# Kernel optimization log

Measured on AMD Instinct MI355X. Metric: run time of the kernel, lower is better.

## Reference

```python
import jax, jax.numpy as jnp
import numpy as np

IMG = 512
SIZES = (16, 32, 64, 128, 256)
FEAT_HW = (128, 64, 32, 16, 8)
STRIDES = tuple(IMG // h for h in FEAT_HW)
RATIOS = np.array([0.5, 1.0, 2.0])
PRE_NMS = 1000        # pre_nms_top_n['testing']
POST_NMS = 300        # post_nms_top_n['testing']
NMS_THRESH = 0.7
MIN_SIZE = 1e-3
BBOX_XFORM_CLIP = float(np.log(1000.0 / 16.0))


def _base_anchors(size):
    h_r = np.sqrt(RATIOS)
    w_r = 1.0 / h_r
    ws = w_r * size
    hs = h_r * size
    return np.round(np.stack([-ws, -hs, ws, hs], axis=1) / 2.0)  # [3,4]


def _level_anchors(size, stride, hw):
    ba = _base_anchors(size)
    s = np.arange(hw, dtype=np.float32) * stride
    yy, xx = np.meshgrid(s, s, indexing='ij')  # y-major like torchvision
    shifts = np.stack([xx.ravel(), yy.ravel(), xx.ravel(), yy.ravel()], axis=1)
    return (shifts[:, None, :] + ba[None, :, :]).reshape(-1, 4).astype(np.float32)


ANCHORS = [jnp.asarray(_level_anchors(SIZES[i], STRIDES[i], FEAT_HW[i])) for i in range(5)]


def _conv(x, w, b, pad):
    y = jax.lax.conv_general_dilated(x, w, (1, 1), [(pad, pad), (pad, pad)],
                                     dimension_numbers=('NCHW', 'OIHW', 'NCHW'))
    return y + b[None, :, None, None]


def _decode(deltas, anchors):
    # deltas [N,K,4], anchors [K,4]; BoxCoder weights (1,1,1,1)
    w = anchors[:, 2] - anchors[:, 0]
    h = anchors[:, 3] - anchors[:, 1]
    cx = anchors[:, 0] + 0.5 * w
    cy = anchors[:, 1] + 0.5 * h
    dx, dy = deltas[..., 0], deltas[..., 1]
    dw = jnp.minimum(deltas[..., 2], BBOX_XFORM_CLIP)
    dh = jnp.minimum(deltas[..., 3], BBOX_XFORM_CLIP)
    pcx = dx * w + cx
    pcy = dy * h + cy
    pw = jnp.exp(dw) * w
    ph = jnp.exp(dh) * h
    return jnp.stack([pcx - 0.5 * pw, pcy - 0.5 * ph,
                      pcx + 0.5 * pw, pcy + 0.5 * ph], axis=-1)


def _nms_single(boxes_off, scores_masked, boxes_raw, scores_raw):
    # greedy NMS over fixed POST_NMS steps; suppressed/invalid score = -1
    def step(s, _):
        i = jnp.argmax(s)
        ok = s[i] > -0.5
        b = boxes_off[i]
        lt = jnp.maximum(b[:2], boxes_off[:, :2])
        rb = jnp.minimum(b[2:], boxes_off[:, 2:])
        wh = jnp.clip(rb - lt, 0.0)
        inter = wh[:, 0] * wh[:, 1]
        area_i = (b[2] - b[0]) * (b[3] - b[1])
        areas = (boxes_off[:, 2] - boxes_off[:, 0]) * (boxes_off[:, 3] - boxes_off[:, 1])
        iou = inter / jnp.maximum(area_i + areas - inter, 1e-9)
        s = jnp.where(ok & (iou > NMS_THRESH), -1.0, s)
        s = s.at[i].set(-1.0)
        return s, (i, ok)

    _, (idx, ok) = jax.lax.scan(step, scores_masked, None, length=POST_NMS)
    out_b = jnp.where(ok[:, None], boxes_raw[idx], 0.0)
    out_s = jnp.where(ok, scores_raw[idx], 0.0)
    return out_b, out_s


def _rpn_forward(feats, conv_w, conv_b, cls_w, cls_b, bbox_w, bbox_b):
    all_s, all_b, lvl_ids = [], [], []
    for lvl, f in enumerate(feats):
        t = jax.nn.relu(_conv(f, conv_w, conv_b, 1))
        obj = _conv(t, cls_w, cls_b, 0)      # [N,3,H,W]
        reg = _conv(t, bbox_w, bbox_b, 0)    # [N,12,H,W]
        N, _, H, W = obj.shape
        obj = obj.transpose(0, 2, 3, 1).reshape(N, -1)  # (H,W,A) order
        reg = reg.reshape(N, 3, 4, H, W).transpose(0, 3, 4, 1, 2).reshape(N, -1, 4)
        boxes = _decode(reg, ANCHORS[lvl])              # [N,HWA,4]
        k = min(PRE_NMS, obj.shape[1])
        top_s, top_i = jax.lax.top_k(obj, k)
        boxes = jnp.take_along_axis(boxes, top_i[:, :, None], axis=1)
        all_s.append(top_s)
        all_b.append(boxes)
        lvl_ids.append(jnp.full((k,), float(lvl), dtype=jnp.float32))
    scores = jnp.concatenate(all_s, axis=1)   # [N,K]
    boxes = jnp.concatenate(all_b, axis=1)    # [N,K,4]
    lvl = jnp.concatenate(lvl_ids)            # [K]
    # clip to image (512x512)
    boxes = jnp.stack([jnp.clip(boxes[..., 0], 0.0, IMG), jnp.clip(boxes[..., 1], 0.0, IMG),
                       jnp.clip(boxes[..., 2], 0.0, IMG), jnp.clip(boxes[..., 3], 0.0, IMG)], axis=-1)
    valid = ((boxes[..., 2] - boxes[..., 0]) >= MIN_SIZE) & ((boxes[..., 3] - boxes[..., 1]) >= MIN_SIZE)
    prob = jax.nn.sigmoid(scores)
    masked = jnp.where(valid, prob, -1.0)
    # batched_nms trick: offset boxes per level so cross-level IoU is 0
    off = lvl * (IMG + 1.0)
    boxes_off = boxes + off[None, :, None]
    return jax.vmap(_nms_single)(boxes_off, masked, boxes, prob)


def setup_inputs() -> dict:
    key = jax.random.key(0)
    ks = jax.random.split(key, 12)
    N, C = 4, 256
    inp = {'images': jax.random.normal(ks[0], (N, 3, IMG, IMG), jnp.float32)}
    for i, hw in enumerate(FEAT_HW):
        inp[f'f{i}'] = jax.random.normal(ks[1 + i], (N, C, hw, hw), jnp.float32)
    inp['conv_w'] = jax.random.normal(ks[6], (C, C, 3, 3), jnp.float32) * 0.01
    inp['conv_b'] = jnp.zeros((C,), jnp.float32)
    inp['cls_w'] = jax.random.normal(ks[7], (3, C, 1, 1), jnp.float32) * 0.01
    inp['cls_b'] = jnp.zeros((3,), jnp.float32)
    inp['bbox_w'] = jax.random.normal(ks[8], (12, C, 1, 1), jnp.float32) * 0.01
    inp['bbox_b'] = jnp.zeros((12,), jnp.float32)
    return inp


def reference(images, f0, f1, f2, f3, f4, conv_w, conv_b, cls_w, cls_b, bbox_w, bbox_b):
    # images only determine the (static) image size used for clipping
    del images
    return _rpn_forward((f0, f1, f2, f3, f4), conv_w, conv_b, cls_w, cls_b, bbox_w, bbox_b)
```

## Files before the change

### kernel.cpp

```cpp
#include <hip/hip_runtime.h>

#define FULL_PER_IMG 65472
#define SEL_PER_IMG  3960
#define BBOX_CLIP    4.135166556742356f

__device__ __forceinline__ unsigned int sortkey(float f){
  unsigned int u = __float_as_uint(f);
  return (u & 0x80000000u) ? ~u : (u | 0x80000000u);
}

__global__ __launch_bounds__(256) void repack_w(const float* __restrict__ src,
                                                float* __restrict__ dst){
  int idx = blockIdx.x*256 + threadIdx.x;
  if (idx >= 589824) return;
  int co = idx & 255;
  int kt = idx >> 8;
  int ci = kt / 9, tap = kt % 9;
  dst[idx] = src[co*2304 + ci*9 + tap];
}

#define CHBUF 1536
#define SMEMF 4160

template<int TX, int H, int NBX>
__device__ void conv_level(int lb,
    const float* __restrict__ f, int strd, float asize, int full_off, float lvl,
    const float* __restrict__ wp, const float* __restrict__ conv_b,
    const float* __restrict__ cls_w, const float* __restrict__ cls_b,
    const float* __restrict__ bbox_w, const float* __restrict__ bbox_b,
    float* __restrict__ A_score, float* __restrict__ A_masked, float* __restrict__ A_boxoff,
    float* smem, float (*s_out)[16])
{
  constexpr int W    = H;
  constexpr int NBY  = H/2;
  constexpr int P    = 2*TX;
  constexpr int ROWW = TX + 4;
  constexpr int CIST = 4*ROWW;
  constexpr int CHFL = 32*CIST;
  constexpr int NSTG = (CHFL + 255)/256;

  const int xb = lb % NBX;
  const int yb = (lb / NBX) % NBY;
  const int n  = lb / (NBX*NBY);
  const int x0 = xb * TX;
  const int y0 = yb * 2;
  const int co = threadIdx.x;
  const float* Fn = f + (size_t)n*256*H*W;
  float* lds_stage = smem;
  float* lds_t     = smem;

  float acc[2][TX];
  #pragma unroll
  for (int o=0;o<2;o++)
    #pragma unroll
    for (int p=0;p<TX;p++) acc[o][p] = conv_b[co];

  int soff[NSTG];
  #pragma unroll
  for (int k=0;k<NSTG;k++){
    const int e  = co + k*256;
    const int cl = e / CIST;
    const int rem = e - cl*CIST;
    const int r  = rem / ROWW;
    const int j  = rem - r*ROWW;
    const int yg = y0 - 1 + r, xg = x0 - 1 + j;
    soff[k] = (e < CHFL && yg>=0 && yg<H && xg>=0 && xg<W)
            ? (cl*H + yg)*W + xg : -1;
  }

#define STAGE(CB, BUF) do {                                                  \
    const float* Fb_ = Fn + (size_t)(CB)*H*W;                                \
    float st_[NSTG];                                                         \
    _Pragma("unroll")                                                        \
    for (int k=0;k<NSTG;k++)                                                 \
      st_[k] = (soff[k] >= 0) ? Fb_[soff[k]] : 0.f;                          \
    _Pragma("unroll")                                                        \
    for (int k=0;k<NSTG;k++){                                                \
      const int e = co + k*256;                                              \
      if (e < CHFL) (BUF)[e] = st_[k];                                       \
    }                                                                        \
  } while(0)

#define CIFMA(SB, CL, WV) do {                                               \
    const float* bp_ = (SB) + (CL)*CIST;                                     \
    _Pragma("unroll")                                                        \
    for (int r=0;r<4;r++){                                                   \
      float rw_[ROWW];                                                       \
      _Pragma("unroll")                                                      \
      for (int q=0;q<ROWW/4;q++){                                            \
        float4 v_ = *(const float4*)(bp_ + r*ROWW + 4*q);                    \
        rw_[4*q+0]=v_.x; rw_[4*q+1]=v_.y;                                    \
        rw_[4*q+2]=v_.z; rw_[4*q+3]=v_.w;                                    \
      }                                                                      \
      if (r <= 2){                                                           \
        _Pragma("unroll")                                                    \
        for (int kx=0;kx<3;kx++){                                            \
          const float w_ = WV[r*3+kx];                                       \
          _Pragma("unroll")                                                  \
          for (int p=0;p<TX;p++) acc[0][p] = fmaf(w_, rw_[p+kx], acc[0][p]); \
        }                                                                    \
      }                                                                      \
      if (r >= 1){                                                           \
        _Pragma("unroll")                                                    \
        for (int kx=0;kx<3;kx++){                                            \
          const float w_ = WV[(r-1)*3+kx];                                   \
          _Pragma("unroll")                                                  \
          for (int p=0;p<TX;p++) acc[1][p] = fmaf(w_, rw_[p+kx], acc[1][p]); \
        }                                                                    \
      }                                                                      \
    }                                                                        \
  } while(0)

  STAGE(0, lds_stage);
  __syncthreads();

  for (int ch=0; ch<8; ++ch){
    const float* sb = lds_stage + (ch&1)*CHBUF;
    for (int cl=0; cl<32; ++cl){
      const int ci = ch*32 + cl;
      float wv[9];
      const float* wrow = wp + (size_t)ci*2304 + co;
      #pragma unroll
      for (int t=0;t<9;t++) wv[t] = wrow[t*256];
      CIFMA(sb, cl, wv);
    }
    if (ch<7){
      STAGE((ch+1)*32, lds_stage + ((ch+1)&1)*CHBUF);
      __syncthreads();
    }
  }
#undef STAGE
#undef CIFMA

  __syncthreads();

  #pragma unroll
  for (int o=0;o<2;o++)
    #pragma unroll
    for (int p=0;p<TX;p++) lds_t[(o*TX+p)*260+co] = fmaxf(acc[o][p], 0.f);
  __syncthreads();

  {
    const int p = threadIdx.x % P;
    const int o = threadIdx.x / P;
    if (o < 15){
      const float* w1 = (o<3) ? (cls_w + o*256) : (bbox_w + (o-3)*256);
      float s = (o<3) ? cls_b[o] : bbox_b[o-3];
      const float4* wl = (const float4*)w1;
      const float4* tl = (const float4*)(lds_t + p*260);
      #pragma unroll 8
      for (int c=0;c<64;c++){
        float4 a = wl[c], b = tl[c];
        s += a.x*b.x + a.y*b.y + a.z*b.z + a.w*b.w;
      }
      s_out[o][p] = s;
    }
  }
  __syncthreads();

  if (threadIdx.x < 3*P){
    const int p = threadIdx.x / 3;
    const int a = threadIdx.x % 3;
    const int px = p % TX;
    const int yo = y0 + p / TX;
    float sraw = s_out[a][p];
    float dx = s_out[3+a*4+0][p];
    float dy = s_out[3+a*4+1][p];
    float dw = fminf(s_out[3+a*4+2][p], BBOX_CLIP);
    float dh = fminf(s_out[3+a*4+3][p], BBOX_CLIP);
    float ratio = (a==0)?0.5f:((a==1)?1.0f:2.0f);
    float hr = sqrtf(ratio);
    float wh2 = rintf(asize / hr * 0.5f);
    float hh2 = rintf(asize * hr * 0.5f);
    float w = 2.f*wh2, h = 2.f*hh2;
    float cx = (float)((x0+px)*strd);
    float cy = (float)(yo*strd);
    float pcx = dx*w + cx, pcy = dy*h + cy;
    float pw = expf(dw)*w, ph = expf(dh)*h;
    float x1 = pcx - 0.5f*pw, y1 = pcy - 0.5f*ph;
    float x2 = pcx + 0.5f*pw, y2 = pcy + 0.5f*ph;
    x1 = fminf(fmaxf(x1,0.f),512.f); y1 = fminf(fmaxf(y1,0.f),512.f);
    x2 = fminf(fmaxf(x2,0.f),512.f); y2 = fminf(fmaxf(y2,0.f),512.f);
    bool valid = ((x2-x1) >= 1e-3f) && ((y2-y1) >= 1e-3f);
    float prob = 1.f/(1.f+expf(-sraw));
    float masked = valid ? prob : -1.f;
    float off = lvl*513.f;
    size_t gi = (size_t)n*FULL_PER_IMG + full_off + ((yo*W + (x0+px))*3 + a);
    A_score[gi]  = sraw;
    A_masked[gi] = masked;
    float4 bo; bo.x=x1+off; bo.y=y1+off; bo.z=x2+off; bo.w=y2+off;
    *(float4*)(A_boxoff + gi*4) = bo;
  }
}

__global__ __launch_bounds__(256)
void conv_all(
    const float* __restrict__ f0, const float* __restrict__ f1,
    const float* __restrict__ f2, const float* __restrict__ f3,
    const float* __restrict__ f4,
    const float* __restrict__ wp, const float* __restrict__ conv_b,
    const float* __restrict__ cls_w, const float* __restrict__ cls_b,
    const float* __restrict__ bbox_w, const float* __restrict__ bbox_b,
    float* __restrict__ A_score, float* __restrict__ A_masked, float* __restrict__ A_boxoff)
{
  __shared__ float smem[SMEMF];
  __shared__ float s_out[15][16];
  const int b = blockIdx.x;
  if (b < 4096)
    conv_level< 8,128,16>(b,      f0,  4,  16.f,     0, 0.f, wp, conv_b, cls_w, cls_b, bbox_w, bbox_b, A_score, A_masked, A_boxoff, smem, s_out);
  else if (b < 5120)
    conv_level< 8, 64, 8>(b-4096, f1,  8,  32.f, 49152, 1.f, wp, conv_b, cls_w, cls_b, bbox_w, bbox_b, A_score, A_masked, A_boxoff, smem, s_out);
  else if (b < 5376)
    conv_level< 8, 32, 4>(b-5120, f2, 16,  64.f, 61440, 2.f, wp, conv_b, cls_w, cls_b, bbox_w, bbox_b, A_score, A_masked, A_boxoff, smem, s_out);
  else if (b < 5504)
    conv_level< 4, 16, 4>(b-5376, f3, 32, 128.f, 64512, 3.f, wp, conv_b, cls_w, cls_b, bbox_w, bbox_b, A_score, A_masked, A_boxoff, smem, s_out);
  else
    conv_level< 4,  8, 2>(b-5504, f4, 64, 256.f, 65280, 4.f, wp, conv_b, cls_w, cls_b, bbox_w, bbox_b, A_score, A_masked, A_boxoff, smem, s_out);
}

__global__ __launch_bounds__(1024) void select_kernel(
    const float* __restrict__ A_score, const float* __restrict__ A_masked,
    const float* __restrict__ A_boxoff,
    float* __restrict__ C_masked, float* __restrict__ C_boxoff)
{
  const int b = blockIdx.x;
  const int tid = threadIdx.x;
  if (b >= 12){
    const int n = b - 12;
    if (tid < 960){
      size_t gF = (size_t)n*FULL_PER_IMG + 64512 + tid;
      size_t gS = (size_t)n*SEL_PER_IMG  + 3000 + tid;
      C_masked[gS] = A_masked[gF];
      *(float4*)(C_boxoff + gS*4) = *(const float4*)(A_boxoff + gF*4);
    }
    return;
  }
  const int n = b / 3, lvl = b % 3;
  const int HWAs[3]  = {49152, 12288, 3072};
  const int FOFF[3]  = {0, 49152, 61440};
  const int HWA = HWAs[lvl];
  const size_t baseF = (size_t)n*FULL_PER_IMG + FOFF[lvl];
  const size_t baseS = (size_t)n*SEL_PER_IMG + lvl*1000;
  const int k = 1000;

  __shared__ unsigned int hist[256];
  __shared__ unsigned int sh_prefix, sh_krem, sh_c0, sh_c1, sh_above;
  if (tid==0){ sh_prefix=0u; sh_krem=(unsigned)k; }
  __syncthreads();

  for (int pass=3; pass>=0; pass--){
    if (tid < 256) hist[tid]=0u;
    __syncthreads();
    unsigned int pfx = sh_prefix;
    for (int i=tid;i<HWA;i+=1024){
      unsigned int u = sortkey(A_score[baseF+i]);
      if (pass==3 || (u >> ((pass+1)*8)) == pfx)
        atomicAdd(&hist[(u>>(pass*8)) & 255u], 1u);
    }
    __syncthreads();
    if (tid==0){
      unsigned int krem = sh_krem, accum = 0u; int chosen = 0;
      for (int bb=255; bb>=0; bb--){
        if (accum + hist[bb] >= krem){ chosen = bb; break; }
        accum += hist[bb];
      }
      sh_krem   = krem - accum;
      sh_prefix = (pfx<<8) | (unsigned)chosen;
    }
    __syncthreads();
  }
  const unsigned int T = sh_prefix;
  if (tid==0){ sh_c0=0u; sh_c1=0u; sh_above = (unsigned)k - sh_krem; }
  __syncthreads();
  const unsigned int nAbove = sh_above, need = sh_krem;

  for (int i=tid;i<HWA;i+=1024){
    unsigned int u = sortkey(A_score[baseF+i]);
    int pos = -1;
    if (u > T) pos = (int)atomicAdd(&sh_c0,1u);
    else if (u == T){
      unsigned int t = atomicAdd(&sh_c1,1u);
      if (t < need) pos = (int)(nAbove + t);
    }
    if (pos >= 0){
      C_masked[baseS+pos] = A_masked[baseF+i];
      *(float4*)(C_boxoff + (baseS+pos)*4) = *(const float4*)(A_boxoff + (baseF+i)*4);
    }
  }
}

__global__ __launch_bounds__(256) void nms_kernel(
    const float* __restrict__ C_masked, const float* __restrict__ C_boxoff,
    float* __restrict__ out_b, float* __restrict__ out_s)
{
  const int n = blockIdx.x, tid = threadIdx.x;
  __shared__ unsigned long long keys[4096];
  __shared__ float accb[304][4];

  #pragma unroll
  for (int s=0; s<16; ++s){
    int i = s*256 + tid;
    unsigned long long kk = 0ull;
    if (i < SEL_PER_IMG){
      unsigned int sk = sortkey(C_masked[(size_t)n*SEL_PER_IMG + i]);
      kk = ((unsigned long long)sk << 32) | (unsigned int)(~(unsigned int)i);
    }
    keys[i] = kk;
  }
  __syncthreads();

  for (int k = 2; k <= 4096; k <<= 1){
    for (int j = k >> 1; j > 0; j >>= 1){
      #pragma unroll
      for (int s=0; s<16; ++s){
        int i = s*256 + tid;
        int ixj = i ^ j;
        if (ixj > i){
          unsigned long long a = keys[i], b = keys[ixj];
          bool up = ((i & k) == 0);
          bool sw = up ? (a < b) : (a > b);
          if (sw){ keys[i] = b; keys[ixj] = a; }
        }
      }
      __syncthreads();
    }
  }

  if (tid >= 64) return;
  const unsigned int THRK = sortkey(-0.5f);
  int nAcc = 0;
  for (int i = 0; i < 4096 && nAcc < 300; ++i){
    unsigned long long kk = keys[i];
    unsigned int khi = (unsigned int)(kk >> 32);
    if (khi <= THRK) break;
    int idx = (int)(~(unsigned int)kk);
    float4 bx = *(const float4*)(C_boxoff + ((size_t)n*SEL_PER_IMG + idx)*4);
    bool sup = false;
    #pragma unroll
    for (int q=0; q<5; ++q){
      int a = tid + q*64;
      if (a < nAcc){
        float a0=accb[a][0], a1=accb[a][1], a2=accb[a][2], a3=accb[a][3];
        float xx1 = fmaxf(a0, bx.x), yy1 = fmaxf(a1, bx.y);
        float xx2 = fminf(a2, bx.z), yy2 = fminf(a3, bx.w);
        float iw = fmaxf(xx2-xx1, 0.f), ih = fmaxf(yy2-yy1, 0.f);
        float inter = iw*ih;
        float ar_a = (a2-a0)*(a3-a1);
        float ar_b = (bx.z-bx.x)*(bx.w-bx.y);
        float iou = inter / fmaxf(ar_a + ar_b - inter, 1e-9f);
        sup |= (iou > 0.7f);
      }
    }
    if (__ballot(sup) == 0ull){
      if (tid == 0){
        accb[nAcc][0]=bx.x; accb[nAcc][1]=bx.y; accb[nAcc][2]=bx.z; accb[nAcc][3]=bx.w;
        int lvl = (idx<1000)?0:((idx<2000)?1:((idx<3000)?2:((idx<3768)?3:4)));
        float off = (float)lvl * 513.f;
        size_t ob = ((size_t)n*300 + nAcc)*4;
        out_b[ob+0]=bx.x-off; out_b[ob+1]=bx.y-off; out_b[ob+2]=bx.z-off; out_b[ob+3]=bx.w-off;
        out_s[(size_t)n*300 + nAcc] = C_masked[(size_t)n*SEL_PER_IMG + idx];
      }
      ++nAcc;
    }
  }
}

extern "C" void kernel_launch(void* const* d_in, const int* in_sizes, int n_in,
                              void* d_out, int out_size, void* d_ws, size_t ws_size,
                              hipStream_t stream) {
  (void)in_sizes; (void)n_in; (void)ws_size;
  const float* f0     = (const float*)d_in[1];
  const float* f1     = (const float*)d_in[2];
  const float* f2     = (const float*)d_in[3];
  const float* f3     = (const float*)d_in[4];
  const float* f4     = (const float*)d_in[5];
  const float* conv_w = (const float*)d_in[6];
  const float* conv_b = (const float*)d_in[7];
  const float* cls_w  = (const float*)d_in[8];
  const float* cls_b  = (const float*)d_in[9];
  const float* bbox_w = (const float*)d_in[10];
  const float* bbox_b = (const float*)d_in[11];

  float* ws       = (float*)d_ws;
  float* wp       = ws;
  float* A_score  = wp       + 589824;
  float* A_masked = A_score  + 261888;
  float* A_boxoff = A_masked + 261888;
  float* C_masked = A_boxoff + 1047552;
  float* C_boxoff = C_masked + 15840;

  float* out_b = (float*)d_out;
  float* out_s = out_b + 4800;

  hipMemsetAsync(d_out, 0, (size_t)out_size*sizeof(float), stream);

  repack_w<<<2304, 256, 0, stream>>>(conv_w, wp);

  conv_all<<<5536, 256, 0, stream>>>(f0, f1, f2, f3, f4,
      wp, conv_b, cls_w, cls_b, bbox_w, bbox_b, A_score, A_masked, A_boxoff);

  select_kernel<<<16, 1024, 0, stream>>>(A_score, A_masked, A_boxoff, C_masked, C_boxoff);
  nms_kernel<<<4, 256, 0, stream>>>(C_masked, C_boxoff, out_b, out_s);
}
```

Baseline: 1.868 ms.

## Pad conv weights for vector loads, privatize select histograms, cache NMS boxes

Conv weights are repacked into a per-(ci,co) record of 12 floats, so each thread reads its 9 taps with two float4 loads plus one scalar instead of nine strided scalar loads. The radix-select kernel gives each wavefront its own histogram and merges them afterwards, which cuts atomic contention. The NMS kernel stages the top 1024 sorted candidate boxes in LDS, prefetches the next box one iteration ahead, and recovers the score from the sort key instead of a global load. The trade-off is that the weight loads are no longer coalesced across adjacent output channels (48-byte stride between lanes) and move a third more bytes, which could hurt the dominant conv kernel.

```diff
diff --git a/kernel.cpp b/kernel.cpp
--- a/kernel.cpp
+++ b/kernel.cpp
@@ -12,11 +12,12 @@
 __global__ __launch_bounds__(256) void repack_w(const float* __restrict__ src,
                                                 float* __restrict__ dst){
   int idx = blockIdx.x*256 + threadIdx.x;
-  if (idx >= 589824) return;
-  int co = idx & 255;
-  int kt = idx >> 8;
-  int ci = kt / 9, tap = kt % 9;
-  dst[idx] = src[co*2304 + ci*9 + tap];
+  if (idx >= 786432) return;
+  int t  = idx % 12;
+  int rc = idx / 12;
+  int co = rc & 255;
+  int ci = rc >> 8;
+  dst[idx] = (t < 9) ? src[co*2304 + ci*9 + t] : 0.f;
 }
 
 #define CHBUF 1536
@@ -118,10 +119,11 @@
     const float* sb = lds_stage + (ch&1)*CHBUF;
     for (int cl=0; cl<32; ++cl){
       const int ci = ch*32 + cl;
-      float wv[9];
-      const float* wrow = wp + (size_t)ci*2304 + co;
-      #pragma unroll
-      for (int t=0;t<9;t++) wv[t] = wrow[t*256];
+      const float* wrow = wp + ((size_t)ci*256 + (size_t)co)*12;
+      float4 wA = *(const float4*)(wrow);
+      float4 wB = *(const float4*)(wrow + 4);
+      float  w8 = wrow[8];
+      float wv[9] = {wA.x,wA.y,wA.z,wA.w, wB.x,wB.y,wB.z,wB.w, w8};
       CIFMA(sb, cl, wv);
     }
     if (ch<7){
@@ -242,27 +244,37 @@
   const size_t baseF = (size_t)n*FULL_PER_IMG + FOFF[lvl];
   const size_t baseS = (size_t)n*SEL_PER_IMG + lvl*1000;
   const int k = 1000;
-
-  __shared__ unsigned int hist[256];
+  const int wid = tid >> 6;
+
+  __shared__ unsigned int hist[16][256];
+  __shared__ unsigned int histM[256];
   __shared__ unsigned int sh_prefix, sh_krem, sh_c0, sh_c1, sh_above;
   if (tid==0){ sh_prefix=0u; sh_krem=(unsigned)k; }
   __syncthreads();
 
   for (int pass=3; pass>=0; pass--){
-    if (tid < 256) hist[tid]=0u;
+    unsigned int* hp = &hist[0][0];
+    for (int z=tid; z<4096; z+=1024) hp[z] = 0u;
     __syncthreads();
     unsigned int pfx = sh_prefix;
     for (int i=tid;i<HWA;i+=1024){
       unsigned int u = sortkey(A_score[baseF+i]);
       if (pass==3 || (u >> ((pass+1)*8)) == pfx)
-        atomicAdd(&hist[(u>>(pass*8)) & 255u], 1u);
+        atomicAdd(&hist[wid][(u>>(pass*8)) & 255u], 1u);
+    }
+    __syncthreads();
+    if (tid < 256){
+      unsigned int s = 0u;
+      #pragma unroll
+      for (int w=0;w<16;w++) s += hist[w][tid];
+      histM[tid] = s;
     }
     __syncthreads();
     if (tid==0){
       unsigned int krem = sh_krem, accum = 0u; int chosen = 0;
       for (int bb=255; bb>=0; bb--){
-        if (accum + hist[bb] >= krem){ chosen = bb; break; }
-        accum += hist[bb];
+        if (accum + histM[bb] >= krem){ chosen = bb; break; }
+        accum += histM[bb];
       }
       sh_krem   = krem - accum;
       sh_prefix = (pfx<<8) | (unsigned)chosen;
@@ -295,6 +307,7 @@
 {
   const int n = blockIdx.x, tid = threadIdx.x;
   __shared__ unsigned long long keys[4096];
+  __shared__ float4 bcache[1024];
   __shared__ float accb[304][4];
 
   #pragma unroll
@@ -326,15 +339,28 @@
     }
   }
 
+  for (int s=tid; s<1024; s+=256){
+    int idx = (int)(~(unsigned int)keys[s]);
+    bcache[s] = *(const float4*)(C_boxoff + ((size_t)n*SEL_PER_IMG + idx)*4);
+  }
+  __syncthreads();
+
   if (tid >= 64) return;
   const unsigned int THRK = sortkey(-0.5f);
   int nAcc = 0;
+  unsigned long long kk = keys[0];
+  float4 bx = bcache[0];
   for (int i = 0; i < 4096 && nAcc < 300; ++i){
-    unsigned long long kk = keys[i];
+    unsigned long long kn = (i+1 < 4096) ? keys[i+1] : 0ull;
+    unsigned int khin = (unsigned int)(kn >> 32);
+    float4 bnext = make_float4(0.f,0.f,0.f,0.f);
+    if (i+1 < 1024) bnext = bcache[i+1];
+    else if (khin > THRK){
+      int idn = (int)(~(unsigned int)kn);
+      bnext = *(const float4*)(C_boxoff + ((size_t)n*SEL_PER_IMG + idn)*4);
+    }
     unsigned int khi = (unsigned int)(kk >> 32);
     if (khi <= THRK) break;
-    int idx = (int)(~(unsigned int)kk);
-    float4 bx = *(const float4*)(C_boxoff + ((size_t)n*SEL_PER_IMG + idx)*4);
     bool sup = false;
     #pragma unroll
     for (int q=0; q<5; ++q){
@@ -354,14 +380,16 @@
     if (__ballot(sup) == 0ull){
       if (tid == 0){
         accb[nAcc][0]=bx.x; accb[nAcc][1]=bx.y; accb[nAcc][2]=bx.z; accb[nAcc][3]=bx.w;
+        int idx = (int)(~(unsigned int)kk);
         int lvl = (idx<1000)?0:((idx<2000)?1:((idx<3000)?2:((idx<3768)?3:4)));
         float off = (float)lvl * 513.f;
         size_t ob = ((size_t)n*300 + nAcc)*4;
         out_b[ob+0]=bx.x-off; out_b[ob+1]=bx.y-off; out_b[ob+2]=bx.z-off; out_b[ob+3]=bx.w-off;
-        out_s[(size_t)n*300 + nAcc] = C_masked[(size_t)n*SEL_PER_IMG + idx];
+        out_s[(size_t)n*300 + nAcc] = __uint_as_float(khi & 0x7fffffffu);
       }
       ++nAcc;
     }
+    kk = kn; bx = bnext;
   }
 }
 
@@ -383,7 +411,7 @@
 
   float* ws       = (float*)d_ws;
   float* wp       = ws;
-  float* A_score  = wp       + 589824;
+  float* A_score  = wp       + 786432;
   float* A_masked = A_score  + 261888;
   float* A_boxoff = A_masked + 261888;
   float* C_masked = A_boxoff + 1047552;
@@ -394,7 +422,7 @@
 
   hipMemsetAsync(d_out, 0, (size_t)out_size*sizeof(float), stream);
 
-  repack_w<<<2304, 256, 0, stream>>>(conv_w, wp);
+  repack_w<<<3072, 256, 0, stream>>>(conv_w, wp);
 
   conv_all<<<5536, 256, 0, stream>>>(f0, f1, f2, f3, f4,
       wp, conv_b, cls_w, cls_b, bbox_w, bbox_b, A_score, A_masked, A_boxoff);
```

Measured after the change: 1.867 ms. Within noise of the previous version (-0.1%).
